# Performance work log

Measured on AMD Instinct MI355X. Metric: run time of the kernel, lower is better.

## Reference

```python
import jax, jax.numpy as jnp
import numpy as np

# token layout: [b, v, T, N, D, t, n, d, f]
B, V, T, TT, N, NN, D, DD, F = 1, 2, 2, 4, 256, 4, 1, 4, 64
OT, OD = 2, 2            # time / depth halo thickness
ATT, H = 128, 32         # att_dim, n_head_channels
NH = ATT // H            # 4 heads
T2, D2 = TT + 2 * OT, DD + 2 * OD


def _ln(x, s, b):
    m = jnp.mean(x, axis=-1, keepdims=True)
    var = jnp.mean((x - m) ** 2, axis=-1, keepdims=True)
    return (x - m) * jax.lax.rsqrt(var + 1e-5) * s + b


def _time_halo(x, o):
    # x: [b,v,T,N,D,t,n,d,f]; copy last/first o intra-window steps from T-neighbors, zeros at edges
    t = x.shape[5]
    prev = jnp.concatenate([jnp.zeros_like(x[:, :, :1]), x[:, :, :-1]], axis=2)
    nxt = jnp.concatenate([x[:, :, 1:], jnp.zeros_like(x[:, :, :1])], axis=2)
    return jnp.concatenate([prev[:, :, :, :, :, t - o:], x, nxt[:, :, :, :, :, :o]], axis=5)


def _depth_halo(x, o):
    d = x.shape[7]
    prev = jnp.concatenate([jnp.zeros_like(x[:, :, :, :, :1]), x[:, :, :, :, :-1]], axis=4)
    nxt = jnp.concatenate([x[:, :, :, :, 1:], jnp.zeros_like(x[:, :, :, :, :1])], axis=4)
    return jnp.concatenate([prev[..., d - o:, :], x, nxt[..., :o, :]], axis=7)


def setup_inputs() -> dict:
    key = jax.random.key(0)
    ks = jax.random.split(key, 6)
    s = 0.02
    return {
        'x': jax.random.normal(ks[0], (B, V, T * TT, N * NN, D * DD, F), jnp.float32),
        'ln1_s': jnp.ones((F,), jnp.float32), 'ln1_b': jnp.zeros((F,), jnp.float32),
        'Wq': jax.random.normal(ks[1], (F, ATT), jnp.float32) * s,
        'Wkv': jax.random.normal(ks[2], (F, 2 * ATT), jnp.float32) * s,
        'bkv': jnp.zeros((2 * ATT,), jnp.float32),
        'Wo': jax.random.normal(ks[3], (ATT, F), jnp.float32) * s,
        'bo': jnp.zeros((F,), jnp.float32),
        'gamma': jnp.full((F,), 1e-2, jnp.float32),
        'ln2_s': jnp.ones((F,), jnp.float32), 'ln2_b': jnp.zeros((F,), jnp.float32),
        'W1': jax.random.normal(ks[4], (F, ATT), jnp.float32) * s,
        'b1': jnp.zeros((ATT,), jnp.float32),
        'W2': jax.random.normal(ks[5], (ATT, F), jnp.float32) * s,
        'b2': jnp.zeros((F,), jnp.float32),
        'gamma_mlp': jnp.full((F,), 1e-2, jnp.float32),
    }


def reference(x, ln1_s, ln1_b, Wq, Wkv, bkv, Wo, bo, gamma, ln2_s, ln2_b, W1, b1, W2, b2, gamma_mlp):
    b = x.shape[0]
    # b v (T t) (N n) (D d) f -> b v T N D t n d f
    tok = x.reshape(b, V, T, TT, N, NN, D, DD, F).transpose(0, 1, 2, 4, 6, 3, 5, 7, 8)
    h = _ln(tok, ln1_s, ln1_b)
    # halo/overlap exchange for kv (time then depth)
    kv_tok = _depth_halo(_time_halo(h, OT), OD)          # [b,v,T,N,D,t2,n,d2,f]
    q = jnp.einsum('bvTNDtndf,fa->bvTNDtnda', h, Wq)
    kvp = jnp.einsum('bvTNDtndf,fa->bvTNDtnda', kv_tok, Wkv) + bkv
    k, v = kvp[..., :ATT], kvp[..., ATT:]
    Sq = V * TT * NN * DD
    Skv = V * T2 * NN * D2
    Wn = b * T * N * D
    # b v T N D t n d (NH H) -> (b T N D) NH (v t n d) H
    def to_att(z, t_, d_, S):
        z = z.reshape(b, V, T, N, D, t_, NN, d_, NH, H)
        z = z.transpose(0, 2, 3, 4, 8, 1, 5, 6, 7, 9)
        return z.reshape(Wn, NH, S, H)
    qr = to_att(q, TT, DD, Sq)
    kr = to_att(k, T2, D2, Skv)
    vr = to_att(v, T2, D2, Skv)
    scores = jnp.einsum('wnqh,wnkh->wnqk', qr, kr) / jnp.sqrt(jnp.float32(H))
    attn = jax.nn.softmax(scores, axis=-1)
    o = jnp.einsum('wnqk,wnkh->wnqh', attn, vr)          # [Wn, NH, Sq, H]
    # reverse to [b,v,T,N,D,t,n,d,att]
    o = o.reshape(b, T, N, D, NH, V, TT, NN, DD, H).transpose(0, 5, 1, 2, 3, 6, 7, 8, 4, 9)
    o = o.reshape(b, V, T, N, D, TT, NN, DD, ATT)
    upd = jnp.einsum('bvTNDtnda,af->bvTNDtndf', o, Wo) + bo
    tok = tok + gamma * upd
    h2 = _ln(tok, ln2_s, ln2_b)
    mlp = jnp.einsum('...f,fa->...a', h2, W1) + b1
    mlp = jnp.einsum('...a,af->...f', jax.nn.gelu(mlp), W2) + b2
    tok = tok + gamma_mlp * mlp
    # b v T N D t n d f -> b v (T t) (N n) (D d) f
    out = tok.transpose(0, 1, 2, 5, 3, 6, 4, 7, 8).reshape(b, V, T * TT, N * NN, D * DD, F)
    return out
```

## Files before the change

kernel.cpp:

```cpp
#include <hip/hip_runtime.h>
#include <math.h>

typedef _Float16 f16;
typedef _Float16 f16x2 __attribute__((ext_vector_type(2)));
typedef _Float16 f16x4 __attribute__((ext_vector_type(4)));
typedef _Float16 f16x8 __attribute__((ext_vector_type(8)));
typedef float f32x4 __attribute__((ext_vector_type(4)));

#if defined(__has_builtin)
#if __has_builtin(__builtin_amdgcn_fdot2)
#define USE_FDOT2 1
#endif
#if __has_builtin(__builtin_amdgcn_exp2f)
#define USE_EXP2 1
#endif
#if __has_builtin(__builtin_amdgcn_cvt_pkrtz)
#define USE_PKRTZ 1
#endif
#endif

__device__ __forceinline__ float fdot2f(f16x2 a, f16x2 b, float c) {
#ifdef USE_FDOT2
    return __builtin_amdgcn_fdot2(a, b, c, false);
#else
    return c + (float)a.x * (float)b.x + (float)a.y * (float)b.y;
#endif
}
__device__ __forceinline__ float exp2fast(float a) {
#ifdef USE_EXP2
    return __builtin_amdgcn_exp2f(a);
#else
    return exp2f(a);
#endif
}
__device__ __forceinline__ f16x2 pk2(float a, float b) {
#ifdef USE_PKRTZ
    auto r0 = __builtin_amdgcn_cvt_pkrtz(a, b);
    f16x2 r; __builtin_memcpy(&r, &r0, 4); return r;
#else
    return (f16x2){(f16)a, (f16)b};
#endif
}
__device__ __forceinline__ int f16x2_as_int(f16x2 v) { int r; __builtin_memcpy(&r, &v, 4); return r; }
__device__ __forceinline__ f16x2 int_as_f16x2(int v) { f16x2 r; __builtin_memcpy(&r, &v, 4); return r; }

namespace {
constexpr int KS  = 40;
constexpr int QLS = 40;
constexpr int VTS = 200;
constexpr int OFF_KL = 0;
constexpr int OFF_VT = 15360;
constexpr int OFF_QL = 28160;
constexpr int ATT_LDS = 38400;
constexpr float C1  = 0.2550600f;
constexpr float CZN = -5.7707801f;
constexpr float CZV = 2.5511480f;

constexpr int FR_WQ  = 0;
constexpr int FR_WKV = 8192;
constexpr int FR_WO  = 24576;
constexpr int FR_W1  = 32768;
constexpr int FR_W2  = 40960;
constexpr int NWF    = 49152;

constexpr int EOLS = 136;
constexpr int ETVS = 66;
constexpr int EH2S = 72;
constexpr int OFF_EOL = 0;
constexpr int OFF_ETV = 17408;
constexpr int OFF_EH2 = 34304;
constexpr int OFF_ERD = 43520;
constexpr int EPI_LDS = 45568;
}

__device__ f16 g_wfrag[NWF];
__device__ f16 g_h[65536 * 64];

__device__ __forceinline__ const f16x8* hfrag(size_t tokblk, int ks, int lg, int lr) {
    return (const f16x8*)(g_h + (((tokblk * 2 + ks) * 4 + lg) * 16 + lr) * 8);
}
__device__ __forceinline__ const f16x8* wfrag(int base, int nks, int ot, int ks, int lg, int lr) {
    return (const f16x8*)(g_wfrag + base + (((ot * nks + ks) * 4 + lg) * 16 + lr) * 8);
}

__global__ void k_conv(const float* __restrict__ Wq, const float* __restrict__ Wkv,
                       const float* __restrict__ Wo, const float* __restrict__ W1,
                       const float* __restrict__ W2) {
    const int i = blockIdx.x * 256 + threadIdx.x;
    const float* src; int IN, OUT, base;
    if (i < FR_WKV)      { src = Wq;  IN = 64;  OUT = 128; base = FR_WQ;  }
    else if (i < FR_WO)  { src = Wkv; IN = 64;  OUT = 256; base = FR_WKV; }
    else if (i < FR_W1)  { src = Wo;  IN = 128; OUT = 64;  base = FR_WO;  }
    else if (i < FR_W2)  { src = W1;  IN = 64;  OUT = 128; base = FR_W1;  }
    else                 { src = W2;  IN = 128; OUT = 64;  base = FR_W2;  }
    const int local = i - base;
    const int j  = local & 7;
    const int lr = (local >> 3) & 15;
    const int lg = (local >> 7) & 3;
    const int nks = IN >> 5;
    const int ks = (local >> 9) & (nks - 1);
    const int ot = local >> (9 + ((nks == 2) ? 1 : 2));
    const int in  = ks * 32 + lg * 8 + j;
    const int out = ot * 16 + lr;
    g_wfrag[i] = (f16)src[in * OUT + out];
}

__global__ __launch_bounds__(256, 8) void k_ln(
    const float* __restrict__ x,
    const float* __restrict__ ln1_s, const float* __restrict__ ln1_b) {
    const int tid = threadIdx.x;
    const size_t tok = (size_t)blockIdx.x * 64 + (tid >> 2);
    const int q = tid & 3;
    const float* xr = x + tok * 64 + q * 16;
    float v[16];
    {
        const float4 a = ((const float4*)xr)[0], b = ((const float4*)xr)[1];
        const float4 c = ((const float4*)xr)[2], d = ((const float4*)xr)[3];
        v[0]=a.x; v[1]=a.y; v[2]=a.z; v[3]=a.w;  v[4]=b.x; v[5]=b.y; v[6]=b.z; v[7]=b.w;
        v[8]=c.x; v[9]=c.y; v[10]=c.z; v[11]=c.w; v[12]=d.x; v[13]=d.y; v[14]=d.z; v[15]=d.w;
    }
    float s = 0.f, ss = 0.f;
    #pragma unroll
    for (int j = 0; j < 16; ++j) { s += v[j]; ss += v[j]*v[j]; }
    s  += __shfl_xor(s, 1);  s  += __shfl_xor(s, 2);
    ss += __shfl_xor(ss, 1); ss += __shfl_xor(ss, 2);
    const float mean = s * 0.015625f;
    const float rstd = rsqrtf(ss * 0.015625f - mean*mean + 1e-5f);
    f16x8 p0, p1;
    #pragma unroll
    for (int j = 0; j < 8; ++j) {
        p0[j] = (f16)((v[j]     - mean) * rstd * ln1_s[q*16 + j]     + ln1_b[q*16 + j]);
        p1[j] = (f16)((v[j + 8] - mean) * rstd * ln1_s[q*16 + j + 8] + ln1_b[q*16 + j + 8]);
    }
    const size_t tokblk = tok >> 4;
    const int lr = (int)(tok & 15);
    const int ks = q >> 1, lg0 = (q & 1) * 2;
    *(f16x8*)(g_h + (((tokblk * 2 + ks) * 4 + lg0) * 16 + lr) * 8)     = p0;
    *(f16x8*)(g_h + (((tokblk * 2 + ks) * 4 + lg0 + 1) * 16 + lr) * 8) = p1;
}

__global__ __launch_bounds__(256, 4) void k_att(
    const float* __restrict__ bkv,
    f16* __restrict__ o_out)
{
    __shared__ __align__(16) char smem[ATT_LDS];
    f16* kl   = (f16*)(smem + OFF_KL);
    f16* vt   = (f16*)(smem + OFF_VT);
    f16* ql   = (f16*)(smem + OFF_QL);

    const int tid  = threadIdx.x;
    const int bid  = blockIdx.x;
    const int w    = bid & 511;
    const int head = bid >> 9;
    const int cb   = head * 32;
    const int n    = w & 255;
    const int t    = w >> 8;

    const int lane = tid & 63, wv = tid >> 6;
    const int lr = lane & 15, lg = lane >> 4;

    {
        #pragma unroll
        for (int mi = 0; mi < 3; ++mi) {
            const int seg = wv * 3 + mi;
            const int v_ = seg / 6;
            const int t2 = (seg % 6) + ((t == 0) ? 2 : 0);
            int tsrc, tt;
            if (t2 < 2)      { tsrc = t - 1; tt = t2 + 2; }
            else if (t2 < 6) { tsrc = t;     tt = t2 - 2; }
            else             { tsrc = t + 1; tt = t2 - 6; }
            const size_t tokblk = (size_t)(v_ * 8 + tsrc * 4 + tt) * 256 + n;
            const int mb = seg * 16;
            #pragma unroll
            for (int nt = 0; nt < 2; ++nt) {
                f32x4 ck = {0.f,0.f,0.f,0.f}, cv = {0.f,0.f,0.f,0.f};
                #pragma unroll
                for (int ks = 0; ks < 2; ++ks) {
                    const f16x8 af = *hfrag(tokblk, ks, lg, lr);
                    const f16x8 bk = *wfrag(FR_WKV, 2, head*2 + nt, ks, lg, lr);
                    const f16x8 bv = *wfrag(FR_WKV, 2, 8 + head*2 + nt, ks, lg, lr);
                    ck = __builtin_amdgcn_mfma_f32_16x16x32_f16(af, bk, ck, 0, 0, 0);
                    cv = __builtin_amdgcn_mfma_f32_16x16x32_f16(af, bv, cv, 0, 0, 0);
                }
                const float bk_b = bkv[cb + nt*16 + lr];
                const float bv_b = bkv[128 + cb + nt*16 + lr];
                #pragma unroll
                for (int e = 0; e < 4; ++e) {
                    const int row = mb + lg*4 + e;
                    kl[row * KS + nt*16 + lr] = (f16)(ck[e] + bk_b);
                    vt[(nt*16 + lr) * VTS + row] = (f16)(cv[e] + bv_b);
                }
            }
        }
        #pragma unroll
        for (int mi = 0; mi < 2; ++mi) {
            const int qm = wv * 2 + mi;
            const int v_ = qm >> 2, tt = qm & 3;
            const size_t tokblk = (size_t)(v_ * 8 + t * 4 + tt) * 256 + n;
            const int qb = v_ * 64 + tt * 16;
            #pragma unroll
            for (int nt = 0; nt < 2; ++nt) {
                f32x4 cq = {0.f,0.f,0.f,0.f};
                #pragma unroll
                for (int ks = 0; ks < 2; ++ks) {
                    const f16x8 af = *hfrag(tokblk, ks, lg, lr);
                    const f16x8 bq = *wfrag(FR_WQ, 2, head*2 + nt, ks, lg, lr);
                    cq = __builtin_amdgcn_mfma_f32_16x16x32_f16(af, bq, cq, 0, 0, 0);
                }
                #pragma unroll
                for (int e = 0; e < 4; ++e)
                    ql[(qb + lg*4 + e) * QLS + nt*16 + lr] = (f16)cq[e];
            }
        }
    }
    __syncthreads();

    const int mA = wv * 32;

    const f16x8 bq0 = *(const f16x8*)(ql + (mA + lr) * QLS + lg * 8);
    const f16x8 bq1 = *(const f16x8*)(ql + (mA + 16 + lr) * QLS + lg * 8);

    f32x4 oc00 = {0.f,0.f,0.f,0.f}, oc01 = {0.f,0.f,0.f,0.f};
    f32x4 oc10 = {0.f,0.f,0.f,0.f}, oc11 = {0.f,0.f,0.f,0.f};
    float l0 = 0.f, l1 = 0.f;

    #pragma unroll 1
    for (int kk = 0; kk < 6; ++kk) {
        const f16x8 ak0 = *(const f16x8*)(kl + (kk*32 + lr) * KS + lg * 8);
        const f16x8 ak1 = *(const f16x8*)(kl + (kk*32 + 16 + lr) * KS + lg * 8);
        const f32x4 ct00 = __builtin_amdgcn_mfma_f32_16x16x32_f16(ak0, bq0, (f32x4){0.f,0.f,0.f,0.f}, 0, 0, 0);
        const f32x4 ct01 = __builtin_amdgcn_mfma_f32_16x16x32_f16(ak0, bq1, (f32x4){0.f,0.f,0.f,0.f}, 0, 0, 0);
        const f32x4 ct10 = __builtin_amdgcn_mfma_f32_16x16x32_f16(ak1, bq0, (f32x4){0.f,0.f,0.f,0.f}, 0, 0, 0);
        const f32x4 ct11 = __builtin_amdgcn_mfma_f32_16x16x32_f16(ak1, bq1, (f32x4){0.f,0.f,0.f,0.f}, 0, 0, 0);

        float p00[4], p01[4], p10[4], p11[4];
        #pragma unroll
        for (int e = 0; e < 4; ++e) {
            p00[e] = exp2fast(fmaf(ct00[e], C1, CZN));
            p01[e] = exp2fast(fmaf(ct01[e], C1, CZN));
            p10[e] = exp2fast(fmaf(ct10[e], C1, CZN));
            p11[e] = exp2fast(fmaf(ct11[e], C1, CZN));
        }
        #pragma unroll
        for (int e = 0; e < 4; ++e) { l0 += p00[e] + p10[e]; l1 += p01[e] + p11[e]; }

        int pk0[4], pk1[4];
        #pragma unroll
        for (int e = 0; e < 4; ++e) {
            pk0[e] = f16x2_as_int(pk2(p00[e], p10[e]));
            pk1[e] = f16x2_as_int(pk2(p01[e], p11[e]));
        }
        f16x8 bp0, bp1;
        #pragma unroll
        for (int j = 0; j < 8; ++j) {
            const int sl = ((lg & 1) * 2 + (j >> 2)) * 16 + lr;
            const f16x2 v0 = int_as_f16x2(__shfl(pk0[j & 3], sl));
            const f16x2 v1 = int_as_f16x2(__shfl(pk1[j & 3], sl));
            bp0[j] = (lg < 2) ? v0.x : v0.y;
            bp1[j] = (lg < 2) ? v1.x : v1.y;
        }

        const f16x8 av0 = *(const f16x8*)(vt + lr * VTS + kk*32 + lg*8);
        const f16x8 av1 = *(const f16x8*)(vt + (16 + lr) * VTS + kk*32 + lg*8);
        oc00 = __builtin_amdgcn_mfma_f32_16x16x32_f16(av0, bp0, oc00, 0, 0, 0);
        oc01 = __builtin_amdgcn_mfma_f32_16x16x32_f16(av0, bp1, oc01, 0, 0, 0);
        oc10 = __builtin_amdgcn_mfma_f32_16x16x32_f16(av1, bp0, oc10, 0, 0, 0);
        oc11 = __builtin_amdgcn_mfma_f32_16x16x32_f16(av1, bp1, oc11, 0, 0, 0);
    }

    l0 += __shfl_xor(l0, 16); l0 += __shfl_xor(l0, 32);
    l1 += __shfl_xor(l1, 16); l1 += __shfl_xor(l1, 32);

    float pz0, pz1;
    {
        const f16x2* qa = (const f16x2*)(ql + (mA + lr) * QLS);
        const f16x2* qb = (const f16x2*)(ql + (mA + 16 + lr) * QLS);
        float sa = 0.f, sb = 0.f;
        #pragma unroll
        for (int j = 0; j < 16; ++j) {
            const float w0 = bkv[cb + 2*j], w1 = bkv[cb + 2*j + 1];
            sa += (float)qa[j].x * w0 + (float)qa[j].y * w1;
            sb += (float)qb[j].x * w0 + (float)qb[j].y * w1;
        }
        pz0 = exp2fast(fmaf(sa, C1, CZV));
        pz1 = exp2fast(fmaf(sb, C1, CZV));
    }
    const float inv0 = 1.0f / (l0 + pz0), pzn0 = pz0 * inv0;
    const float inv1 = 1.0f / (l1 + pz1), pzn1 = pz1 * inv1;

    #define EPI_TILE(CC, MT, QT, INVQ, PZQ) { \
        const int q = mA + (QT) * 16 + lr; \
        const int v2 = q >> 6, tt2 = (q >> 4) & 3, nn2 = (q >> 2) & 3, dd2 = q & 3; \
        const size_t tk = ((size_t)(v2 * 8 + t * 4 + tt2) * 1024 + n * 4 + nn2) * 4 + dd2; \
        _Pragma("unroll") \
        for (int e = 0; e < 4; ++e) { \
            const int ch = (MT) * 16 + lg * 4 + e; \
            const float oo = fmaf(PZQ, bkv[128 + cb + ch], CC[e] * (INVQ)); \
            o_out[tk * 128 + cb + ch] = (f16)oo; \
        } }
    EPI_TILE(oc00, 0, 0, inv0, pzn0)
    EPI_TILE(oc01, 0, 1, inv1, pzn1)
    EPI_TILE(oc10, 1, 0, inv0, pzn0)
    EPI_TILE(oc11, 1, 1, inv1, pzn1)
    #undef EPI_TILE
}

__global__ __launch_bounds__(256, 3) void k_epi(
    const float* __restrict__ x, const f16* __restrict__ o_in,
    const float* __restrict__ bo, const float* __restrict__ gamma,
    const float* __restrict__ ln2_s, const float* __restrict__ ln2_b,
    const float* __restrict__ b1, const float* __restrict__ b2,
    const float* __restrict__ gm, float* __restrict__ out)
{
    __shared__ __align__(16) char smem[EPI_LDS];
    f16* eol    = (f16*)(smem + OFF_EOL);
    float* etv  = (float*)(smem + OFF_ETV);
    f16* eh2    = (f16*)(smem + OFF_EH2);
    float* erd  = (float*)(smem + OFF_ERD);
    f16* ehid   = eol;

    const int tid = threadIdx.x;
    const int lane = tid & 63, wv = tid >> 6;
    const int lr = lane & 15, lg = lane >> 4;
    const int mb = wv * 16;
    const size_t tok0 = (size_t)blockIdx.x * 64;

    {
        const int tk = tid >> 2, part = tid & 3;
        const f16x8* src = (const f16x8*)(o_in + (tok0 + tk) * 128 + part * 32);
        f16x8* dst = (f16x8*)(eol + tk * EOLS + part * 32);
        dst[0] = src[0]; dst[1] = src[1]; dst[2] = src[2]; dst[3] = src[3];
    }
    __syncthreads();

    {
        f16x8 a_[4];
        #pragma unroll
        for (int ks = 0; ks < 4; ++ks)
            a_[ks] = *(const f16x8*)(eol + (mb + lr) * EOLS + ks*32 + lg*8);
        #pragma unroll
        for (int nt = 0; nt < 4; ++nt) {
            const int ch = nt * 16 + lr;
            f32x4 c = {0.f,0.f,0.f,0.f};
            #pragma unroll
            for (int ks = 0; ks < 4; ++ks)
                c = __builtin_amdgcn_mfma_f32_16x16x32_f16(a_[ks], *wfrag(FR_WO, 4, nt, ks, lg, lr), c, 0, 0, 0);
            const float bo_c = bo[ch], ga_c = gamma[ch];
            #pragma unroll
            for (int e = 0; e < 4; ++e) {
                const int tk = mb + lg*4 + e;
                etv[tk * ETVS + ch] = x[(tok0 + tk)*64 + ch] + ga_c * (c[e] + bo_c);
            }
        }
    }
    __syncthreads();

    {
        const int tk = tid >> 2, q = tid & 3;
        const float* tr = etv + tk * ETVS + q * 16;
        float s1 = 0.f, s2 = 0.f;
        #pragma unroll
        for (int j = 0; j < 16; ++j) { const float v = tr[j]; s1 += v; s2 += v*v; }
        erd[(tk*4 + q)*2] = s1; erd[(tk*4 + q)*2 + 1] = s2;
    }
    __syncthreads();
    {
        const int tk = tid >> 2, q = tid & 3;
        float a1 = 0.f, a2 = 0.f;
        #pragma unroll
        for (int i = 0; i < 4; ++i) { a1 += erd[(tk*4 + i)*2]; a2 += erd[(tk*4 + i)*2 + 1]; }
        const float mean = a1 * 0.015625f;
        const float rstd = rsqrtf(a2 * 0.015625f - mean*mean + 1e-5f);
        const float* tr = etv + tk * ETVS + q * 16;
        f16* hr = eh2 + tk * EH2S + q * 16;
        #pragma unroll
        for (int j = 0; j < 16; ++j)
            hr[j] = (f16)((tr[j]-mean)*rstd*ln2_s[q*16 + j] + ln2_b[q*16 + j]);
    }
    __syncthreads();

    {
        f16x8 a_[2];
        #pragma unroll
        for (int ks = 0; ks < 2; ++ks)
            a_[ks] = *(const f16x8*)(eh2 + (mb + lr) * EH2S + ks*32 + lg*8);
        #pragma unroll
        for (int nt = 0; nt < 8; ++nt) {
            const int ch = nt * 16 + lr;
            f32x4 c = {0.f,0.f,0.f,0.f};
            #pragma unroll
            for (int ks = 0; ks < 2; ++ks)
                c = __builtin_amdgcn_mfma_f32_16x16x32_f16(a_[ks], *wfrag(FR_W1, 2, nt, ks, lg, lr), c, 0, 0, 0);
            const float b1_c = b1[ch];
            #pragma unroll
            for (int e = 0; e < 4; ++e) {
                const int tk = mb + lg*4 + e;
                const float z = c[e] + b1_c;
                const float u = 0.7978845608028654f * (z + 0.044715f * z*z*z);
                ehid[tk * EOLS + ch] = (f16)(z / (1.0f + exp2fast(-2.8853900817779268f * u)));
            }
        }
    }
    __syncthreads();

    {
        f16x8 a_[4];
        #pragma unroll
        for (int ks = 0; ks < 4; ++ks)
            a_[ks] = *(const f16x8*)(ehid + (mb + lr) * EOLS + ks*32 + lg*8);
        #pragma unroll
        for (int nt = 0; nt < 4; ++nt) {
            const int ch = nt * 16 + lr;
            f32x4 c = {0.f,0.f,0.f,0.f};
            #pragma unroll
            for (int ks = 0; ks < 4; ++ks)
                c = __builtin_amdgcn_mfma_f32_16x16x32_f16(a_[ks], *wfrag(FR_W2, 4, nt, ks, lg, lr), c, 0, 0, 0);
            const float b2_c = b2[ch], gm_c = gm[ch];
            #pragma unroll
            for (int e = 0; e < 4; ++e) {
                const int tk = mb + lg*4 + e;
                out[(tok0 + tk)*64 + ch] = etv[tk * ETVS + ch] + gm_c * (c[e] + b2_c);
            }
        }
    }
}

extern "C" void kernel_launch(void* const* d_in, const int* in_sizes, int n_in,
                              void* d_out, int out_size, void* d_ws, size_t ws_size,
                              hipStream_t stream) {
    const float* x        = (const float*)d_in[0];
    const float* ln1_s    = (const float*)d_in[1];
    const float* ln1_b    = (const float*)d_in[2];
    const float* Wq       = (const float*)d_in[3];
    const float* Wkv      = (const float*)d_in[4];
    const float* bkv      = (const float*)d_in[5];
    const float* Wo       = (const float*)d_in[6];
    const float* bo       = (const float*)d_in[7];
    const float* gamma    = (const float*)d_in[8];
    const float* ln2_s    = (const float*)d_in[9];
    const float* ln2_b    = (const float*)d_in[10];
    const float* W1       = (const float*)d_in[11];
    const float* b1       = (const float*)d_in[12];
    const float* W2       = (const float*)d_in[13];
    const float* b2       = (const float*)d_in[14];
    const float* gamma_mlp= (const float*)d_in[15];

    f16* o_buf = (f16*)d_out;
    float* out = (float*)d_out;

    hipLaunchKernelGGL(k_conv, dim3(NWF / 256), dim3(256), 0, stream,
                       Wq, Wkv, Wo, W1, W2);
    hipLaunchKernelGGL(k_ln, dim3(1024), dim3(256), 0, stream,
                       x, ln1_s, ln1_b);
    hipLaunchKernelGGL(k_att, dim3(2048), dim3(256), 0, stream,
                       bkv, o_buf);
    hipLaunchKernelGGL(k_epi, dim3(1024), dim3(256), 0, stream,
                       x, o_buf, bo, gamma, ln2_s, ln2_b, b1, b2, gamma_mlp, out);
}
```

Baseline: 59.46 us.

## Keep Q fragments in registers via shuffles, merge conv and LN kernels

Q projection results are now repacked across lanes with shuffles straight into the MFMA B-operand layout, so the Q LDS buffer goes away. That shrinks shared memory from 38400 to 28160 bytes and raises the launch-bounds occupancy hint from 4 to 5 blocks. The softmax zero-key term is now computed from the register fragments with cross-lane reductions. Separately, the weight-conversion kernel and the LayerNorm kernel are merged into one launch using block-index dispatch. Trade-offs: more shuffle instructions and register pressure, and a tighter register budget from the higher occupancy target.

```diff
diff --git a/kernel.cpp b/kernel.cpp
--- a/kernel.cpp
+++ b/kernel.cpp
@@ -46,12 +46,10 @@
 
 namespace {
 constexpr int KS  = 40;
-constexpr int QLS = 40;
 constexpr int VTS = 200;
 constexpr int OFF_KL = 0;
 constexpr int OFF_VT = 15360;
-constexpr int OFF_QL = 28160;
-constexpr int ATT_LDS = 38400;
+constexpr int ATT_LDS = 28160;
 constexpr float C1  = 0.2550600f;
 constexpr float CZN = -5.7707801f;
 constexpr float CZV = 2.5511480f;
@@ -62,6 +60,7 @@
 constexpr int FR_W1  = 32768;
 constexpr int FR_W2  = 40960;
 constexpr int NWF    = 49152;
+constexpr int CONV_BLOCKS = NWF / 256;
 
 constexpr int EOLS = 136;
 constexpr int ETVS = 66;
@@ -83,33 +82,36 @@
     return (const f16x8*)(g_wfrag + base + (((ot * nks + ks) * 4 + lg) * 16 + lr) * 8);
 }
 
-__global__ void k_conv(const float* __restrict__ Wq, const float* __restrict__ Wkv,
-                       const float* __restrict__ Wo, const float* __restrict__ W1,
-                       const float* __restrict__ W2) {
-    const int i = blockIdx.x * 256 + threadIdx.x;
-    const float* src; int IN, OUT, base;
-    if (i < FR_WKV)      { src = Wq;  IN = 64;  OUT = 128; base = FR_WQ;  }
-    else if (i < FR_WO)  { src = Wkv; IN = 64;  OUT = 256; base = FR_WKV; }
-    else if (i < FR_W1)  { src = Wo;  IN = 128; OUT = 64;  base = FR_WO;  }
-    else if (i < FR_W2)  { src = W1;  IN = 64;  OUT = 128; base = FR_W1;  }
-    else                 { src = W2;  IN = 128; OUT = 64;  base = FR_W2;  }
-    const int local = i - base;
-    const int j  = local & 7;
-    const int lr = (local >> 3) & 15;
-    const int lg = (local >> 7) & 3;
-    const int nks = IN >> 5;
-    const int ks = (local >> 9) & (nks - 1);
-    const int ot = local >> (9 + ((nks == 2) ? 1 : 2));
-    const int in  = ks * 32 + lg * 8 + j;
-    const int out = ot * 16 + lr;
-    g_wfrag[i] = (f16)src[in * OUT + out];
-}
-
-__global__ __launch_bounds__(256, 8) void k_ln(
+__global__ __launch_bounds__(256, 8) void k_convln(
+    const float* __restrict__ Wq, const float* __restrict__ Wkv,
+    const float* __restrict__ Wo, const float* __restrict__ W1,
+    const float* __restrict__ W2,
     const float* __restrict__ x,
     const float* __restrict__ ln1_s, const float* __restrict__ ln1_b) {
+    const int bid = blockIdx.x;
+    if (bid < CONV_BLOCKS) {
+        const int i = bid * 256 + threadIdx.x;
+        const float* src; int IN, OUT, base;
+        if (i < FR_WKV)      { src = Wq;  IN = 64;  OUT = 128; base = FR_WQ;  }
+        else if (i < FR_WO)  { src = Wkv; IN = 64;  OUT = 256; base = FR_WKV; }
+        else if (i < FR_W1)  { src = Wo;  IN = 128; OUT = 64;  base = FR_WO;  }
+        else if (i < FR_W2)  { src = W1;  IN = 64;  OUT = 128; base = FR_W1;  }
+        else                 { src = W2;  IN = 128; OUT = 64;  base = FR_W2;  }
+        const int local = i - base;
+        const int j  = local & 7;
+        const int lr = (local >> 3) & 15;
+        const int lg = (local >> 7) & 3;
+        const int nks = IN >> 5;
+        const int ks = (local >> 9) & (nks - 1);
+        const int ot = local >> (9 + ((nks == 2) ? 1 : 2));
+        const int in  = ks * 32 + lg * 8 + j;
+        const int out = ot * 16 + lr;
+        g_wfrag[i] = (f16)src[in * OUT + out];
+        return;
+    }
+    const int lb = bid - CONV_BLOCKS;
     const int tid = threadIdx.x;
-    const size_t tok = (size_t)blockIdx.x * 64 + (tid >> 2);
+    const size_t tok = (size_t)lb * 64 + (tid >> 2);
     const int q = tid & 3;
     const float* xr = x + tok * 64 + q * 16;
     float v[16];
@@ -139,14 +141,13 @@
     *(f16x8*)(g_h + (((tokblk * 2 + ks) * 4 + lg0 + 1) * 16 + lr) * 8) = p1;
 }
 
-__global__ __launch_bounds__(256, 4) void k_att(
+__global__ __launch_bounds__(256, 5) void k_att(
     const float* __restrict__ bkv,
     f16* __restrict__ o_out)
 {
     __shared__ __align__(16) char smem[ATT_LDS];
     f16* kl   = (f16*)(smem + OFF_KL);
     f16* vt   = (f16*)(smem + OFF_VT);
-    f16* ql   = (f16*)(smem + OFF_QL);
 
     const int tid  = threadIdx.x;
     const int bid  = blockIdx.x;
@@ -158,7 +159,9 @@
 
     const int lane = tid & 63, wv = tid >> 6;
     const int lr = lane & 15, lg = lane >> 4;
-
+    const int mA = wv * 32;
+
+    f16x8 bq0, bq1;
     {
         #pragma unroll
         for (int mi = 0; mi < 3; ++mi) {
@@ -197,7 +200,7 @@
             const int qm = wv * 2 + mi;
             const int v_ = qm >> 2, tt = qm & 3;
             const size_t tokblk = (size_t)(v_ * 8 + t * 4 + tt) * 256 + n;
-            const int qb = v_ * 64 + tt * 16;
+            int pkA[2], pkB[2];
             #pragma unroll
             for (int nt = 0; nt < 2; ++nt) {
                 f32x4 cq = {0.f,0.f,0.f,0.f};
@@ -207,18 +210,40 @@
                     const f16x8 bq = *wfrag(FR_WQ, 2, head*2 + nt, ks, lg, lr);
                     cq = __builtin_amdgcn_mfma_f32_16x16x32_f16(af, bq, cq, 0, 0, 0);
                 }
-                #pragma unroll
-                for (int e = 0; e < 4; ++e)
-                    ql[(qb + lg*4 + e) * QLS + nt*16 + lr] = (f16)cq[e];
-            }
-        }
-    }
-    __syncthreads();
-
-    const int mA = wv * 32;
-
-    const f16x8 bq0 = *(const f16x8*)(ql + (mA + lr) * QLS + lg * 8);
-    const f16x8 bq1 = *(const f16x8*)(ql + (mA + 16 + lr) * QLS + lg * 8);
+                pkA[nt] = f16x2_as_int(pk2(cq[0], cq[1]));
+                pkB[nt] = f16x2_as_int(pk2(cq[2], cq[3]));
+            }
+            f16x8 bq_;
+            #pragma unroll
+            for (int j = 0; j < 8; ++j) {
+                const int sl = (lr >> 2) * 16 + (lg & 1) * 8 + j;
+                const int a0 = __shfl(pkA[0], sl), b0 = __shfl(pkB[0], sl);
+                const int a1 = __shfl(pkA[1], sl), b1 = __shfl(pkB[1], sl);
+                const int s0 = (lr & 2) ? b0 : a0;
+                const int s1 = (lr & 2) ? b1 : a1;
+                const f16x2 vv = int_as_f16x2((lg >= 2) ? s1 : s0);
+                bq_[j] = (lr & 1) ? vv.y : vv.x;
+            }
+            if (mi == 0) bq0 = bq_; else bq1 = bq_;
+        }
+    }
+
+    float pz0, pz1;
+    {
+        float s0 = 0.f, s1 = 0.f;
+        #pragma unroll
+        for (int j = 0; j < 8; ++j) {
+            const float wgt = bkv[cb + lg*8 + j];
+            s0 += (float)bq0[j] * wgt;
+            s1 += (float)bq1[j] * wgt;
+        }
+        s0 += __shfl_xor(s0, 16); s0 += __shfl_xor(s0, 32);
+        s1 += __shfl_xor(s1, 16); s1 += __shfl_xor(s1, 32);
+        pz0 = exp2fast(fmaf(s0, C1, CZV));
+        pz1 = exp2fast(fmaf(s1, C1, CZV));
+    }
+
+    __syncthreads();
 
     f32x4 oc00 = {0.f,0.f,0.f,0.f}, oc01 = {0.f,0.f,0.f,0.f};
     f32x4 oc10 = {0.f,0.f,0.f,0.f}, oc11 = {0.f,0.f,0.f,0.f};
@@ -271,20 +296,6 @@
     l0 += __shfl_xor(l0, 16); l0 += __shfl_xor(l0, 32);
     l1 += __shfl_xor(l1, 16); l1 += __shfl_xor(l1, 32);
 
-    float pz0, pz1;
-    {
-        const f16x2* qa = (const f16x2*)(ql + (mA + lr) * QLS);
-        const f16x2* qb = (const f16x2*)(ql + (mA + 16 + lr) * QLS);
-        float sa = 0.f, sb = 0.f;
-        #pragma unroll
-        for (int j = 0; j < 16; ++j) {
-            const float w0 = bkv[cb + 2*j], w1 = bkv[cb + 2*j + 1];
-            sa += (float)qa[j].x * w0 + (float)qa[j].y * w1;
-            sb += (float)qb[j].x * w0 + (float)qb[j].y * w1;
-        }
-        pz0 = exp2fast(fmaf(sa, C1, CZV));
-        pz1 = exp2fast(fmaf(sb, C1, CZV));
-    }
     const float inv0 = 1.0f / (l0 + pz0), pzn0 = pz0 * inv0;
     const float inv1 = 1.0f / (l1 + pz1), pzn1 = pz1 * inv1;
 
@@ -448,10 +459,8 @@
     f16* o_buf = (f16*)d_out;
     float* out = (float*)d_out;
 
-    hipLaunchKernelGGL(k_conv, dim3(NWF / 256), dim3(256), 0, stream,
-                       Wq, Wkv, Wo, W1, W2);
-    hipLaunchKernelGGL(k_ln, dim3(1024), dim3(256), 0, stream,
-                       x, ln1_s, ln1_b);
+    hipLaunchKernelGGL(k_convln, dim3(CONV_BLOCKS + 1024), dim3(256), 0, stream,
+                       Wq, Wkv, Wo, W1, W2, x, ln1_s, ln1_b);
     hipLaunchKernelGGL(k_att, dim3(2048), dim3(256), 0, stream,
                        bkv, o_buf);
     hipLaunchKernelGGL(k_epi, dim3(1024), dim3(256), 0, stream,
```

Result: faster. 55.97 us (-5.9%).
